# Performance work log

Measured on AMD Instinct MI355X. Metric: run time of the kernel, lower is better.

Reference implementation:

```python
import jax, jax.numpy as jnp
import numpy as np

NS = 6   # stuff classes
NT = 4   # thing classes
B, N, H, W, ROI = 2, 32, 768, 768, 28
C = NS + NT
NEG = -100.0


def setup_inputs():
    key = jax.random.key(0)
    k1, k2, k3, k4, k5, k6, k7 = jax.random.split(key, 7)
    sem_logits = jax.random.normal(k1, (B, C, H, W), dtype=jnp.float32)
    roi_msk_logits = jax.random.normal(k2, (B, N, NT, ROI, ROI), dtype=jnp.float32)
    y0 = jax.random.uniform(k3, (B, N), minval=0.0, maxval=H - 240.0)
    x0 = jax.random.uniform(k4, (B, N), minval=0.0, maxval=W - 240.0)
    hb = jax.random.uniform(k5, (B, N), minval=40.0, maxval=200.0)
    wb = jax.random.uniform(k6, (B, N), minval=40.0, maxval=200.0)
    bbx = jnp.stack([y0, x0, y0 + hb, x0 + wb], axis=-1).astype(jnp.float32)
    cls = jax.random.randint(k7, (B, N), 0, NT, dtype=jnp.int32)
    return {"sem_logits": sem_logits, "roi_msk_logits": roi_msk_logits, "bbx": bbx, "cls": cls}


def _fuse_logits(sem_logits, roi_msk_logits, bbx, cls):
    """Float part of Pofusion_ONNX.forward -> po_logits [B, NS+N, H, W]."""
    Bb, Cc, Hh, Ww = sem_logits.shape
    Nn = bbx.shape[1]
    R = roi_msk_logits.shape[-1]
    yy = jnp.arange(Hh)
    xx = jnp.arange(Ww)
    # per-box mask logits of its predicted class: [B,N,R,R]
    msk = jnp.take_along_axis(roi_msk_logits, cls[:, :, None, None, None], axis=2)[:, :, 0]
    stuff = sem_logits[:, :NS]  # [B,NS,H,W]
    y0 = jnp.floor(bbx[..., 0]).astype(jnp.int32)
    x0 = jnp.floor(bbx[..., 1]).astype(jnp.int32)
    y1 = jnp.floor(bbx[..., 2]).astype(jnp.int32)
    x1 = jnp.floor(bbx[..., 3]).astype(jnp.int32)
    # ---- po_process_semantic_logits: instance canvas (uses round()+1 on max corner) ----
    y1r = (jnp.round(bbx[..., 2]) + 1.0).astype(jnp.int32)
    x1r = (jnp.round(bbx[..., 3]) + 1.0).astype(jnp.int32)
    in_y_s = (yy[None, None, :] >= y0[..., None]) & (yy[None, None, :] < y1r[..., None])  # [B,N,H]
    in_x_s = (xx[None, None, :] >= x0[..., None]) & (xx[None, None, :] < x1r[..., None])  # [B,N,W]
    thing_logit = jnp.take_along_axis(sem_logits, (cls + NS)[:, :, None, None], axis=1)   # [B,N,H,W]
    inst = jnp.where(in_y_s[:, :, :, None] & in_x_s[:, :, None, :], thing_logit, NEG)
    # ---- po_process_mask_logits: bilinear resize (align_corners=False) + paste ----
    h = jnp.maximum(y1 - y0 + 1, 1).astype(jnp.float32)
    w = jnp.maximum(x1 - x0 + 1, 1).astype(jnp.float32)
    ys = jnp.maximum(y0, 0); ye = jnp.minimum(y1 + 1, Hh)
    xs = jnp.maximum(x0, 0); xe = jnp.minimum(x1 + 1, Ww)
    in_y_m = (yy[None, None, :] >= ys[..., None]) & (yy[None, None, :] < ye[..., None])
    in_x_m = (xx[None, None, :] >= xs[..., None]) & (xx[None, None, :] < xe[..., None])
    # source coords, PyTorch half-pixel convention with lower clamp at 0
    sy = (yy[None, None, :].astype(jnp.float32) - y0[..., None] + 0.5) * (R / h[..., None]) - 0.5
    sx = (xx[None, None, :].astype(jnp.float32) - x0[..., None] + 0.5) * (R / w[..., None]) - 0.5
    sy = jnp.clip(sy, 0.0, R - 1.0)
    sx = jnp.clip(sx, 0.0, R - 1.0)
    iy0 = jnp.floor(sy).astype(jnp.int32); iy1 = jnp.minimum(iy0 + 1, R - 1); wy = sy - iy0
    ix0 = jnp.floor(sx).astype(jnp.int32); ix1 = jnp.minimum(ix0 + 1, R - 1); wx = sx - ix0
    # separable bilinear: rows first (cheap [B,N,H,R] intermediate), then columns
    m0 = jnp.take_along_axis(msk, iy0[:, :, :, None], axis=2)
    m1 = jnp.take_along_axis(msk, iy1[:, :, :, None], axis=2)
    m_y = m0 * (1.0 - wy[..., None]) + m1 * wy[..., None]          # [B,N,H,R]
    c0 = jnp.take_along_axis(m_y, ix0[:, :, None, :], axis=3)
    c1 = jnp.take_along_axis(m_y, ix1[:, :, None, :], axis=3)
    resized = c0 * (1.0 - wx[:, :, None, :]) + c1 * wx[:, :, None, :]  # [B,N,H,W]
    mask_canvas = jnp.where(in_y_m[:, :, :, None] & in_x_m[:, :, None, :], resized, NEG)
    combined = (jax.nn.sigmoid(inst) + jax.nn.sigmoid(mask_canvas)) * (inst + mask_canvas)
    return jnp.concatenate([stuff, combined], axis=1)  # [B, NS+N, H, W]


def _post(po_logits, sem_logits, cls):
    """po_assign_class_label + po_generate_seamless_output (min_stuff_area=0)."""
    b3 = jnp.arange(B)[:, None, None]
    b2 = jnp.arange(B)[:, None]
    po_pred = jnp.argmax(po_logits, axis=1)   # argmax(softmax) == argmax(logits)
    sem_pred = jnp.argmax(sem_logits, axis=1)
    thing = po_pred >= NS
    k = jnp.clip(po_pred - NS, 0, N - 1)      # instance (box) id per pixel
    # per-instance histogram of sem_pred over its region (regions are disjoint)
    hist = jnp.zeros((B, N, C), jnp.int32).at[b3, k, sem_pred].add(thing.astype(jnp.int32))
    total = hist.sum(-1)
    present = total > 0
    sem_max = jnp.argmax(hist, axis=-1).astype(jnp.int32)  # first max == torch unique order
    max_cnt = hist.max(-1)
    tmp = cls + NS
    br1 = sem_max == tmp
    br2 = (~br1) & (2 * max_cnt >= total) & (sem_max < NS) & present  # max/total >= 0.5
    sem_label = jnp.where(br2, sem_max, tmp)
    kept = present & ~br2
    idx = jnp.cumsum(present.astype(jnp.int32), axis=1) - 1  # rank among present ids
    inst_label = jnp.where(kept, idx, -1)
    po_sem = jnp.where(thing, sem_label[b3, k], po_pred.astype(jnp.int32))
    po_inst = jnp.where(thing, inst_label[b3, k], -1)
    # ---- seamless output ----
    sp = jnp.zeros((B, NS), jnp.int32).at[b3, jnp.clip(po_sem, 0, NS - 1)].add((po_sem < NS).astype(jnp.int32))
    stuff_present = sp > 0
    stuff_rank = jnp.cumsum(stuff_present.astype(jnp.int32), axis=1) - 1
    n_stuff = stuff_present.sum(1).astype(jnp.int32)  # [B]
    v = jnp.where(kept, idx, N)
    present_v = (jnp.zeros((B, N + 1), jnp.int32).at[b2, v].add(1) > 0)[:, :N]
    rank_v = jnp.cumsum(present_v.astype(jnp.int32), axis=1) - 1
    seam_inst = 1 + n_stuff[:, None, None] + rank_v[b3, jnp.clip(po_inst, 0, N - 1)]
    seam_stuff = stuff_rank[b3, jnp.clip(po_sem, 0, NS - 1)] + 1
    seam = jnp.where(po_inst >= 0, seam_inst, jnp.where(po_sem < NS, seam_stuff, 0))
    po_pred_seamless = seam.reshape(B * H, W).astype(jnp.int32)  # torch cat over batch
    # padded class list [255, sorted stuff classes..., kept instance classes...]
    L = 1 + NS + N
    po_cls = jnp.full((B, L + 1), -1, jnp.int32).at[:, 0].set(255)
    stuff_pos = jnp.where(stuff_present, 1 + stuff_rank, L)  # L = dump slot
    po_cls = po_cls.at[b2, stuff_pos].set(jnp.broadcast_to(jnp.arange(NS, dtype=jnp.int32), (B, NS)))
    rank_k = jnp.cumsum(kept.astype(jnp.int32), axis=1) - 1
    inst_pos = jnp.where(kept, 1 + n_stuff[:, None] + rank_k, L)
    po_cls = po_cls.at[b2, inst_pos].set(tmp)
    po_cls = po_cls[:, :L]
    valid_len = (1 + n_stuff + kept.sum(1)).astype(jnp.int32)
    po_iscrowd = jnp.where(jnp.arange(L)[None, :] < valid_len[:, None], 0, -1).astype(jnp.int32)
    return po_pred_seamless, po_cls, po_iscrowd, valid_len


def reference(sem_logits, roi_msk_logits, bbx, cls):
    po_logits = _fuse_logits(sem_logits, roi_msk_logits, bbx, cls)
    return _post(po_logits, sem_logits, cls)
```

## Files before the change

kernel.cpp:

```cpp
#include <hip/hip_runtime.h>
#include <math.h>

#define NSs 6
#define NTs 4
#define Bb  2
#define Nn  32
#define Hh  768
#define Ww  768
#define Rr  28
#define Cch 10
#define NCH 38
#define HW  (Hh*Ww)
#define NEGD (-100.0)
#define NKEY (Nn*Cch + NSs)

struct InstP {
  int y0, x0, y1r, x1r;
  int ys, ye, xs, xe;
  float sc_y, sc_x;
  int tc;
  int mskoff;
};

__device__ __forceinline__ double sigd(double x) { return 1.0 / (1.0 + exp(-x)); }

__global__ void k_zero(int* __restrict__ p, int n) {
  for (int i = threadIdx.x; i < n; i += 256) p[i] = 0;
}

__device__ __forceinline__ void do_px(
    int b, int y, int x, const float (&ch)[Cch], unsigned rel,
    const InstP* __restrict__ spar, const float* __restrict__ roi,
    int* __restrict__ out_pred, int* __restrict__ s_all, double EPS)
{
  int smp = 0; float smv = ch[0];
#pragma unroll
  for (int c = 1; c < Cch; c++) if (ch[c] > smv) { smv = ch[c]; smp = c; }

  double m = (double)ch[0]; int pidx = 0;
#pragma unroll
  for (int c = 1; c < NSs; c++) { double v = (double)ch[c]; if (v > m) { m = v; pidx = c; } }

  int next_ch = NSs;
  while (rel) {
    int n = __ffs(rel) - 1; rel &= rel - 1;
    int chn_ = NSs + n;
    if (chn_ > next_ch && EPS > m) { m = EPS; pidx = next_ch; }
    next_ch = chn_ + 1;
    const InstP p = spar[n];
    bool in_i = (y >= p.y0) && (y < p.y1r) && (x >= p.x0) && (x < p.x1r);
    bool in_m = (y >= p.ys) && (y < p.ye)  && (x >= p.xs) && (x < p.xe);
    bool in_any = in_i || in_m;
    if (__any(in_any)) {
      if (in_any) {
        int tcl = p.tc;
        float tl = (tcl == 6) ? ch[6] : (tcl == 7) ? ch[7] : (tcl == 8) ? ch[8] : ch[9];
        double iv = in_i ? (double)tl : NEGD;
        double mv = NEGD;
        if (in_m) {
          double syv = ((double)(y - p.y0) + 0.5) * (double)p.sc_y - 0.5;
          double sxv = ((double)(x - p.x0) + 0.5) * (double)p.sc_x - 0.5;
          syv = fmin(fmax(syv, 0.0), 27.0);
          sxv = fmin(fmax(sxv, 0.0), 27.0);
          int iy0 = (int)syv, ix0 = (int)sxv;
          int iy1 = min(iy0 + 1, 27), ix1 = min(ix0 + 1, 27);
          double wy = syv - (double)iy0, wx = sxv - (double)ix0;
          const float* mp = roi + p.mskoff;
          double m00 = (double)mp[iy0*Rr + ix0];
          double m01 = (double)mp[iy0*Rr + ix1];
          double m10 = (double)mp[iy1*Rr + ix0];
          double m11 = (double)mp[iy1*Rr + ix1];
          double c0 = m00*(1.0 - wy) + m10*wy;
          double c1 = m01*(1.0 - wy) + m11*wy;
          mv = c0*(1.0 - wx) + c1*wx;
        }
        double s2 = iv + mv;
        if (fmax(2.0*s2, 0.0) > m) {
          double val = (sigd(iv) + sigd(mv)) * s2;
          if (val > m) { m = val; pidx = chn_; }
        }
      } else {
        if (EPS > m) { m = EPS; pidx = chn_; }
      }
    } else {
      if (EPS > m) { m = EPS; pidx = chn_; }
    }
  }
  if (next_ch < NCH && EPS > m) { m = EPS; pidx = next_ch; }

  out_pred[(size_t)b*HW + (size_t)y*Ww + x] = pidx;
  int key = (pidx >= NSs) ? ((pidx - NSs)*Cch + smp) : (Nn*Cch + pidx);
  atomicAdd(&s_all[key], 1);
}

__global__ __launch_bounds__(256) void k_fuse(
    const float* __restrict__ sem, const float* __restrict__ roi,
    const float* __restrict__ bbx, const int* __restrict__ cls,
    int* __restrict__ out_pred, int* __restrict__ g_hist, int* __restrict__ g_scount)
{
  __shared__ InstP spar[Nn];
  __shared__ int s_all[NKEY];
  __shared__ unsigned s_rel;

  const int bid = blockIdx.x;
  const int y   = bid % Hh;
  const int b   = bid / Hh;
  const int tid = threadIdx.x;

  if (tid == 0) s_rel = 0u;
  for (int i = tid; i < NKEY; i += 256) s_all[i] = 0;
  if (tid < Nn) {
    const int n = tid;
    const float* bbp = bbx + ((size_t)b*Nn + n)*4;
    float f0 = bbp[0], f1 = bbp[1], f2 = bbp[2], f3 = bbp[3];
    int y0 = (int)floorf(f0), x0 = (int)floorf(f1);
    int y1 = (int)floorf(f2), x1 = (int)floorf(f3);
    int y1r = (int)(rintf(f2) + 1.0f);
    int x1r = (int)(rintf(f3) + 1.0f);
    float hh = fmaxf((float)(y1 - y0 + 1), 1.0f);
    float wd = fmaxf((float)(x1 - x0 + 1), 1.0f);
    InstP p;
    p.y0 = y0; p.x0 = x0; p.y1r = y1r; p.x1r = x1r;
    p.ys = max(y0, 0); p.ye = min(y1 + 1, Hh);
    p.xs = max(x0, 0); p.xe = min(x1 + 1, Ww);
    p.sc_y = 28.0f / hh; p.sc_x = 28.0f / wd;
    int cl = cls[b*Nn + n];
    p.tc = NSs + cl;
    p.mskoff = (((b*Nn + n)*NTs) + cl)*Rr*Rr;
    spar[n] = p;
    bool rowi = (y >= y0)   && (y < y1r);
    bool rowm = (y >= p.ys) && (y < p.ye);
    if (rowi || rowm) atomicOr(&s_rel, 1u << n);
  }
  __syncthreads();

  const double EPS = (sigd(NEGD) + sigd(NEGD)) * (NEGD + NEGD);
  const float* base = sem + (size_t)b*Cch*HW + (size_t)y*Ww;

  float ch0[Cch], ch1[Cch], ch2[Cch];
#pragma unroll
  for (int c = 0; c < Cch; c++) ch0[c] = base[(size_t)c*HW + tid];
#pragma unroll
  for (int c = 0; c < Cch; c++) ch1[c] = base[(size_t)c*HW + tid + 256];
#pragma unroll
  for (int c = 0; c < Cch; c++) ch2[c] = base[(size_t)c*HW + tid + 512];

  const unsigned rel = s_rel;
  do_px(b, y, tid,       ch0, rel, spar, roi, out_pred, s_all, EPS);
  do_px(b, y, tid + 256, ch1, rel, spar, roi, out_pred, s_all, EPS);
  do_px(b, y, tid + 512, ch2, rel, spar, roi, out_pred, s_all, EPS);

  __syncthreads();
  for (int i = tid; i < NKEY; i += 256) {
    int v = s_all[i];
    if (v) {
      if (i < Nn*Cch) atomicAdd(&g_hist[b*Nn*Cch + i], v);
      else            atomicAdd(&g_scount[b*NSs + (i - Nn*Cch)], v);
    }
  }
}

__global__ __launch_bounds__(128) void k_post(
    const int* __restrict__ g_hist, const int* __restrict__ g_scount,
    const int* __restrict__ cls, int* __restrict__ lut,
    int* __restrict__ out_tail)
{
  __shared__ int sh[Bb*Nn*Cch];
  __shared__ int spc_s[Bb][NSs];
  __shared__ int pcs[Bb][40];
  const int t = threadIdx.x;
  for (int i = t; i < Bb*Nn*Cch; i += 128) sh[i] = g_hist[i];
  if (t < Bb*NSs) spc_s[t/NSs][t%NSs] = g_scount[t];
  __syncthreads();

  const int b    = t >> 6;
  const int lane = t & 63;
  const bool act = lane < Nn;

  int total = 0, mi = 0, mx = -1, tmp = 0;
  bool br2 = false, kept = false;
  if (act) {
    const int* hb = sh + b*Nn*Cch + lane*Cch;
#pragma unroll
    for (int c = 0; c < Cch; c++) { int v = hb[c]; total += v; if (v > mx) { mx = v; mi = c; } }
    tmp = cls[b*Nn + lane] + NSs;
    bool present = total > 0;
    bool b1 = (mi == tmp);
    br2  = (!b1) && (2*mx >= total) && (mi < NSs) && present;
    kept = present && !br2;
    if (br2) atomicAdd(&spc_s[b][mi], total);
  }
  __syncthreads();

  unsigned mask6 = (unsigned)(__ballot(lane < NSs && spc_s[b][lane] > 0) & 0x3Full);
  int nstuff = __popc(mask6);
  unsigned kmask = (unsigned)(__ballot(act && kept) & 0xFFFFFFFFull);
  int nk = __popc(kmask);
  int vlen = 1 + nstuff + nk;

  if (lane < NSs) lut[b*NCH + lane] = __popc(mask6 & ((1u << lane) - 1)) + 1;
  if (act) {
    int rk     = __popc(kmask & ((1u << lane) - 1));
    int srk_mi = __popc(mask6 & ((1u << mi) - 1));
    lut[b*NCH + NSs + lane] = kept ? (1 + nstuff + rk) : (br2 ? srk_mi + 1 : 0);
  }

  if (lane < 39) pcs[b][lane] = -1;
  __syncthreads();
  if (lane == 0) pcs[b][0] = 255;
  if (lane < NSs && ((mask6 >> lane) & 1))
    pcs[b][1 + __popc(mask6 & ((1u << lane) - 1))] = lane;
  if (act && kept)
    pcs[b][1 + nstuff + __popc(kmask & ((1u << lane) - 1))] = tmp;
  __syncthreads();

  int* pc = out_tail;
  int* ic = out_tail + Bb*39;
  int* vl = out_tail + 2*Bb*39;
  if (lane < 39) {
    pc[b*39 + lane] = pcs[b][lane];
    ic[b*39 + lane] = (lane < vlen) ? 0 : -1;
  }
  if (lane == 0) vl[b] = vlen;
}

__global__ __launch_bounds__(256) void k_seam(int* __restrict__ pred, const int* __restrict__ lut)
{
  __shared__ int slut[Bb*NCH];
  int tid = threadIdx.x;
  if (tid < Bb*NCH) slut[tid] = lut[tid];
  __syncthreads();
  size_t i = ((size_t)blockIdx.x*256 + tid) * 4;
  int b = (int)(i / HW);
  int4 v = *reinterpret_cast<int4*>(pred + i);
  int base = b*NCH;
  v.x = slut[base + v.x];
  v.y = slut[base + v.y];
  v.z = slut[base + v.z];
  v.w = slut[base + v.w];
  *reinterpret_cast<int4*>(pred + i) = v;
}

extern "C" void kernel_launch(void* const* d_in, const int* in_sizes, int n_in,
                              void* d_out, int out_size, void* d_ws, size_t ws_size,
                              hipStream_t stream)
{
  const float* sem = (const float*)d_in[0];
  const float* roi = (const float*)d_in[1];
  const float* bbx = (const float*)d_in[2];
  const int*   cls = (const int*)d_in[3];
  int* out = (int*)d_out;

  int* g_hist   = (int*)d_ws;
  int* g_scount = g_hist + Bb*Nn*Cch;
  int* lut      = g_scount + Bb*NSs;

  k_zero<<<1, 256, 0, stream>>>(g_hist, Bb*Nn*Cch + Bb*NSs);
  k_fuse<<<dim3(Bb*Hh), 256, 0, stream>>>(sem, roi, bbx, cls, out, g_hist, g_scount);
  k_post<<<1, 128, 0, stream>>>(g_hist, g_scount, cls, lut, out + (size_t)Bb*HW);
  k_seam<<<dim3((Bb*HW)/(256*4)), 256, 0, stream>>>(out, lut);
}
```

Before: 113.1 us.

## Fuse all stages into one cooperative persistent kernel with grid syncs

Replaces the four-launch pipeline (zero, fuse, post, seam) with a single cooperative kernel of 512 blocks, each handling three rows. Each block keeps its per-pixel class indices in shared memory as bytes and writes per-block histograms to workspace. After a grid sync, block 0 reduces the histograms and builds the LUT, and after a second grid sync every block applies the LUT straight from shared memory. This removes the launch gaps and the global read-modify-write of the prediction map, at the cost of two grid-wide barriers, a serial reduction in one block, and lower parallelism (512 blocks) under launch_bounds(256,2). The old four-kernel path remains as a fallback if the cooperative launch is not possible.

```diff
diff --git a/kernel.cpp b/kernel.cpp
--- a/kernel.cpp
+++ b/kernel.cpp
@@ -1,5 +1,8 @@
 #include <hip/hip_runtime.h>
+#include <hip/hip_cooperative_groups.h>
 #include <math.h>
+
+namespace cg = cooperative_groups;
 
 #define NSs 6
 #define NTs 4
@@ -13,6 +16,7 @@
 #define HW  (Hh*Ww)
 #define NEGD (-100.0)
 #define NKEY (Nn*Cch + NSs)
+#define WS_LUT (Bb*NKEY*256)
 
 struct InstP {
   int y0, x0, y1r, x1r;
@@ -24,18 +28,15 @@
 
 __device__ __forceinline__ double sigd(double x) { return 1.0 / (1.0 + exp(-x)); }
 
-__global__ void k_zero(int* __restrict__ p, int n) {
-  for (int i = threadIdx.x; i < n; i += 256) p[i] = 0;
-}
-
-__device__ __forceinline__ void do_px(
-    int b, int y, int x, const float (&ch)[Cch], unsigned rel,
+__device__ __forceinline__ int fuse_px(
+    int y, int x, const float (&ch)[Cch], unsigned rel,
     const InstP* __restrict__ spar, const float* __restrict__ roi,
-    int* __restrict__ out_pred, int* __restrict__ s_all, double EPS)
+    double EPS, int* smp_out)
 {
   int smp = 0; float smv = ch[0];
 #pragma unroll
   for (int c = 1; c < Cch; c++) if (ch[c] > smv) { smv = ch[c]; smp = c; }
+  *smp_out = smp;
 
   double m = (double)ch[0]; int pidx = 0;
 #pragma unroll
@@ -87,10 +88,184 @@
     }
   }
   if (next_ch < NCH && EPS > m) { m = EPS; pidx = next_ch; }
-
-  out_pred[(size_t)b*HW + (size_t)y*Ww + x] = pidx;
-  int key = (pidx >= NSs) ? ((pidx - NSs)*Cch + smp) : (Nn*Cch + pidx);
-  atomicAdd(&s_all[key], 1);
+  return pidx;
+}
+
+__device__ __forceinline__ void setup_inst(
+    int b, int tid, const float* __restrict__ bbx, const int* __restrict__ cls,
+    InstP* spar)
+{
+  const int n = tid;
+  const float* bbp = bbx + ((size_t)b*Nn + n)*4;
+  float f0 = bbp[0], f1 = bbp[1], f2 = bbp[2], f3 = bbp[3];
+  int y0 = (int)floorf(f0), x0 = (int)floorf(f1);
+  int y1 = (int)floorf(f2), x1 = (int)floorf(f3);
+  int y1r = (int)(rintf(f2) + 1.0f);
+  int x1r = (int)(rintf(f3) + 1.0f);
+  float hh = fmaxf((float)(y1 - y0 + 1), 1.0f);
+  float wd = fmaxf((float)(x1 - x0 + 1), 1.0f);
+  InstP p;
+  p.y0 = y0; p.x0 = x0; p.y1r = y1r; p.x1r = x1r;
+  p.ys = max(y0, 0); p.ye = min(y1 + 1, Hh);
+  p.xs = max(x0, 0); p.xe = min(x1 + 1, Ww);
+  p.sc_y = 28.0f / hh; p.sc_x = 28.0f / wd;
+  int cl = cls[b*Nn + n];
+  p.tc = NSs + cl;
+  p.mskoff = (((b*Nn + n)*NTs) + cl)*Rr*Rr;
+  spar[n] = p;
+}
+
+__global__ __launch_bounds__(256, 2) void k_all(
+    const float* __restrict__ sem, const float* __restrict__ roi,
+    const float* __restrict__ bbx, const int* __restrict__ cls,
+    int* __restrict__ out, int* __restrict__ ws)
+{
+  __shared__ InstP spar[Nn];
+  __shared__ int s_all[NKEY];
+  __shared__ unsigned s_relrow[3];
+  __shared__ unsigned char s_pidx8[3*Ww];
+  __shared__ int s_red[Bb*NKEY];
+  __shared__ int s_spc[Bb][NSs];
+  __shared__ int s_pcs[Bb][40];
+  __shared__ int slut[NCH];
+
+  cg::grid_group grid = cg::this_grid();
+
+  const int bid = blockIdx.x;
+  const int b   = bid >> 8;
+  const int j   = bid & 255;
+  const int y0b = j * 3;
+  const int tid = threadIdx.x;
+
+  if (tid < 3) s_relrow[tid] = 0u;
+  for (int i = tid; i < NKEY; i += 256) s_all[i] = 0;
+  if (tid < Nn) {
+    setup_inst(b, tid, bbx, cls, spar);
+    const InstP p = spar[tid];
+#pragma unroll
+    for (int r = 0; r < 3; r++) {
+      int y = y0b + r;
+      bool rowi = (y >= p.y0) && (y < p.y1r);
+      bool rowm = (y >= p.ys) && (y < p.ye);
+      if (rowi || rowm) atomicOr(&s_relrow[r], 1u << tid);
+    }
+  }
+  __syncthreads();
+
+  const double EPS = (sigd(NEGD) + sigd(NEGD)) * (NEGD + NEGD);
+  const float* base = sem + (size_t)b*Cch*HW + (size_t)y0b*Ww;
+  unsigned rel[3];
+#pragma unroll
+  for (int r = 0; r < 3; r++) rel[r] = s_relrow[r];
+
+  float cur[3][Cch], nxt[3][Cch];
+#pragma unroll
+  for (int r = 0; r < 3; r++)
+#pragma unroll
+    for (int c = 0; c < Cch; c++) cur[r][c] = base[(size_t)c*HW + (size_t)r*Ww + tid];
+
+  for (int ck = 0; ck < 3; ck++) {
+    const int x = ck*256 + tid;
+    if (ck < 2) {
+#pragma unroll
+      for (int r = 0; r < 3; r++)
+#pragma unroll
+        for (int c = 0; c < Cch; c++) nxt[r][c] = base[(size_t)c*HW + (size_t)r*Ww + x + 256];
+    }
+#pragma unroll
+    for (int r = 0; r < 3; r++) {
+      int smp;
+      int pidx = fuse_px(y0b + r, x, cur[r], rel[r], spar, roi, EPS, &smp);
+      s_pidx8[r*Ww + x] = (unsigned char)pidx;
+      int key = (pidx >= NSs) ? ((pidx - NSs)*Cch + smp) : (Nn*Cch + pidx);
+      atomicAdd(&s_all[key], 1);
+    }
+    if (ck < 2) {
+#pragma unroll
+      for (int r = 0; r < 3; r++)
+#pragma unroll
+        for (int c = 0; c < Cch; c++) cur[r][c] = nxt[r][c];
+    }
+  }
+  __syncthreads();
+  for (int i = tid; i < NKEY; i += 256) ws[(b*NKEY + i)*256 + j] = s_all[i];
+  __threadfence();
+  grid.sync();
+
+  if (bid == 0) {
+    const int w = tid >> 6, lane = tid & 63;
+    for (int k = w; k < Bb*NKEY; k += 4) {
+      int s = 0;
+#pragma unroll
+      for (int q = 0; q < 4; q++) s += ws[k*256 + q*64 + lane];
+#pragma unroll
+      for (int off = 32; off; off >>= 1) s += __shfl_down(s, off, 64);
+      if (lane == 0) s_red[k] = s;
+    }
+    __syncthreads();
+    const int b2 = w;
+    const bool bv = b2 < Bb;
+    const bool act = bv && (lane < Nn);
+    if (bv && lane < NSs) s_spc[b2][lane] = s_red[b2*NKEY + Nn*Cch + lane];
+    __syncthreads();
+    int total = 0, mi = 0, mx = -1, tmpv = 0;
+    bool br2f = false, keptf = false;
+    if (act) {
+      const int* hb = &s_red[b2*NKEY + lane*Cch];
+#pragma unroll
+      for (int c = 0; c < Cch; c++) { int v = hb[c]; total += v; if (v > mx) { mx = v; mi = c; } }
+      tmpv = cls[b2*Nn + lane] + NSs;
+      bool present = total > 0;
+      bool b1 = (mi == tmpv);
+      br2f  = (!b1) && (2*mx >= total) && (mi < NSs) && present;
+      keptf = present && !br2f;
+      if (br2f) atomicAdd(&s_spc[b2][mi], total);
+    }
+    __syncthreads();
+    bool pred6 = bv && (lane < NSs) && (s_spc[b2 & 1][lane] > 0);
+    unsigned mask6 = (unsigned)(__ballot(pred6) & 0x3Full);
+    int nstuff = __popc(mask6);
+    unsigned kmask = (unsigned)(__ballot(act && keptf) & 0xFFFFFFFFull);
+    int nk = __popc(kmask);
+    int vlen = 1 + nstuff + nk;
+
+    if (bv && lane < NSs)
+      ws[WS_LUT + b2*NCH + lane] = __popc(mask6 & ((1u << lane) - 1)) + 1;
+    if (act) {
+      int rk  = __popc(kmask & ((1u << lane) - 1));
+      int srk = __popc(mask6 & ((1u << mi) - 1));
+      ws[WS_LUT + b2*NCH + NSs + lane] = keptf ? (1 + nstuff + rk) : (br2f ? srk + 1 : 0);
+    }
+    if (bv && lane < 39) s_pcs[b2][lane] = -1;
+    __syncthreads();
+    if (bv && lane == 0) s_pcs[b2][0] = 255;
+    if (pred6) s_pcs[b2][1 + __popc(mask6 & ((1u << lane) - 1))] = lane;
+    if (act && keptf) s_pcs[b2][1 + nstuff + __popc(kmask & ((1u << lane) - 1))] = tmpv;
+    __syncthreads();
+    int* pc = out + (size_t)Bb*HW;
+    int* ic = pc + Bb*39;
+    int* vl = ic + Bb*39;
+    if (bv && lane < 39) {
+      pc[b2*39 + lane] = s_pcs[b2][lane];
+      ic[b2*39 + lane] = (lane < vlen) ? 0 : -1;
+    }
+    if (bv && lane == 0) vl[b2] = vlen;
+  }
+  __threadfence();
+  grid.sync();
+
+  if (tid < NCH) slut[tid] = ws[WS_LUT + b*NCH + tid];
+  __syncthreads();
+#pragma unroll
+  for (int r = 0; r < 3; r++)
+    for (int ck = 0; ck < 3; ck++) {
+      int x = ck*256 + tid;
+      out[(size_t)b*HW + (size_t)(y0b + r)*Ww + x] = slut[s_pidx8[r*Ww + x]];
+    }
+}
+
+__global__ void k_zero(int* __restrict__ p, int n) {
+  for (int i = threadIdx.x; i < n; i += 256) p[i] = 0;
 }
 
 __global__ __launch_bounds__(256) void k_fuse(
@@ -110,27 +285,11 @@
   if (tid == 0) s_rel = 0u;
   for (int i = tid; i < NKEY; i += 256) s_all[i] = 0;
   if (tid < Nn) {
-    const int n = tid;
-    const float* bbp = bbx + ((size_t)b*Nn + n)*4;
-    float f0 = bbp[0], f1 = bbp[1], f2 = bbp[2], f3 = bbp[3];
-    int y0 = (int)floorf(f0), x0 = (int)floorf(f1);
-    int y1 = (int)floorf(f2), x1 = (int)floorf(f3);
-    int y1r = (int)(rintf(f2) + 1.0f);
-    int x1r = (int)(rintf(f3) + 1.0f);
-    float hh = fmaxf((float)(y1 - y0 + 1), 1.0f);
-    float wd = fmaxf((float)(x1 - x0 + 1), 1.0f);
-    InstP p;
-    p.y0 = y0; p.x0 = x0; p.y1r = y1r; p.x1r = x1r;
-    p.ys = max(y0, 0); p.ye = min(y1 + 1, Hh);
-    p.xs = max(x0, 0); p.xe = min(x1 + 1, Ww);
-    p.sc_y = 28.0f / hh; p.sc_x = 28.0f / wd;
-    int cl = cls[b*Nn + n];
-    p.tc = NSs + cl;
-    p.mskoff = (((b*Nn + n)*NTs) + cl)*Rr*Rr;
-    spar[n] = p;
-    bool rowi = (y >= y0)   && (y < y1r);
+    setup_inst(b, tid, bbx, cls, spar);
+    const InstP p = spar[tid];
+    bool rowi = (y >= p.y0) && (y < p.y1r);
     bool rowm = (y >= p.ys) && (y < p.ye);
-    if (rowi || rowm) atomicOr(&s_rel, 1u << n);
+    if (rowi || rowm) atomicOr(&s_rel, 1u << tid);
   }
   __syncthreads();
 
@@ -146,9 +305,16 @@
   for (int c = 0; c < Cch; c++) ch2[c] = base[(size_t)c*HW + tid + 512];
 
   const unsigned rel = s_rel;
-  do_px(b, y, tid,       ch0, rel, spar, roi, out_pred, s_all, EPS);
-  do_px(b, y, tid + 256, ch1, rel, spar, roi, out_pred, s_all, EPS);
-  do_px(b, y, tid + 512, ch2, rel, spar, roi, out_pred, s_all, EPS);
+  int smp, pidx;
+  pidx = fuse_px(y, tid, ch0, rel, spar, roi, EPS, &smp);
+  out_pred[(size_t)b*HW + (size_t)y*Ww + tid] = pidx;
+  atomicAdd(&s_all[(pidx >= NSs) ? ((pidx - NSs)*Cch + smp) : (Nn*Cch + pidx)], 1);
+  pidx = fuse_px(y, tid + 256, ch1, rel, spar, roi, EPS, &smp);
+  out_pred[(size_t)b*HW + (size_t)y*Ww + tid + 256] = pidx;
+  atomicAdd(&s_all[(pidx >= NSs) ? ((pidx - NSs)*Cch + smp) : (Nn*Cch + pidx)], 1);
+  pidx = fuse_px(y, tid + 512, ch2, rel, spar, roi, EPS, &smp);
+  out_pred[(size_t)b*HW + (size_t)y*Ww + tid + 512] = pidx;
+  atomicAdd(&s_all[(pidx >= NSs) ? ((pidx - NSs)*Cch + smp) : (Nn*Cch + pidx)], 1);
 
   __syncthreads();
   for (int i = tid; i < NKEY; i += 256) {
@@ -250,13 +416,25 @@
   const float* bbx = (const float*)d_in[2];
   const int*   cls = (const int*)d_in[3];
   int* out = (int*)d_out;
-
-  int* g_hist   = (int*)d_ws;
-  int* g_scount = g_hist + Bb*Nn*Cch;
-  int* lut      = g_scount + Bb*NSs;
-
-  k_zero<<<1, 256, 0, stream>>>(g_hist, Bb*Nn*Cch + Bb*NSs);
-  k_fuse<<<dim3(Bb*Hh), 256, 0, stream>>>(sem, roi, bbx, cls, out, g_hist, g_scount);
-  k_post<<<1, 128, 0, stream>>>(g_hist, g_scount, cls, lut, out + (size_t)Bb*HW);
-  k_seam<<<dim3((Bb*HW)/(256*4)), 256, 0, stream>>>(out, lut);
-}
+  int* wsI = (int*)d_ws;
+
+  int maxB = 0;
+  hipError_t e = hipOccupancyMaxActiveBlocksPerMultiprocessor(
+      &maxB, (const void*)k_all, 256, 0);
+  bool ok = (e == hipSuccess) && (maxB >= 2) && (ws_size >= (size_t)(WS_LUT + Bb*NCH)*4);
+  if (ok) {
+    void* args[] = { (void*)&sem, (void*)&roi, (void*)&bbx, (void*)&cls,
+                     (void*)&out, (void*)&wsI };
+    ok = hipLaunchCooperativeKernel((const void*)k_all, dim3(512), dim3(256),
+                                    args, 0, stream) == hipSuccess;
+  }
+  if (!ok) {
+    int* g_hist   = wsI;
+    int* g_scount = g_hist + Bb*Nn*Cch;
+    int* lut      = g_scount + Bb*NSs;
+    k_zero<<<1, 256, 0, stream>>>(g_hist, Bb*Nn*Cch + Bb*NSs);
+    k_fuse<<<dim3(Bb*Hh), 256, 0, stream>>>(sem, roi, bbx, cls, out, g_hist, g_scount);
+    k_post<<<1, 128, 0, stream>>>(g_hist, g_scount, cls, lut, out + (size_t)Bb*HW);
+    k_seam<<<dim3((Bb*HW)/(256*4)), 256, 0, stream>>>(out, lut);
+  }
+}
```

Result: slower. 383.9 us (+239.5%).
